# Optimization experiments

Hardware: AMD Instinct MI355X
Metric: run time of the kernel (lower is better)

## Reference

```python
import jax, jax.numpy as jnp
import numpy as np

HALF = 24576          # per-side HalfKP features (64 king sq * 6 piece * 64 sq)
NUMEL = 2 * HALF      # util.half_kp_numel()
BASE = 128
B = 8192


def _linear(x, W, b):
    return x @ W.T + b


def setup_inputs() -> dict:
    key = jax.random.key(0)
    ks = jax.random.split(key, 16)
    s = 0.01
    return {
        "pov": jax.random.uniform(ks[0], (B, 1), dtype=jnp.float32),
        "white": jax.random.uniform(ks[1], (B, HALF), dtype=jnp.float32),
        "black": jax.random.uniform(ks[2], (B, HALF), dtype=jnp.float32),
        "w_aff_W": jax.random.normal(ks[3], (BASE, NUMEL), dtype=jnp.float32) * s,
        "w_aff_b": jax.random.normal(ks[4], (BASE,), dtype=jnp.float32) * s,
        "b_aff_W": jax.random.normal(ks[5], (BASE, NUMEL), dtype=jnp.float32) * s,
        "b_aff_b": jax.random.normal(ks[6], (BASE,), dtype=jnp.float32) * s,
        "fc0_W": jax.random.normal(ks[7], (32, 2 * BASE), dtype=jnp.float32) * s,
        "fc0_b": jax.random.normal(ks[8], (32,), dtype=jnp.float32) * s,
        "fc1_W": jax.random.normal(ks[9], (32, 32), dtype=jnp.float32) * s,
        "fc1_b": jax.random.normal(ks[10], (32,), dtype=jnp.float32) * s,
        "fc2_W": jax.random.normal(ks[11], (32, 64), dtype=jnp.float32) * s,
        "fc2_b": jax.random.normal(ks[12], (32,), dtype=jnp.float32) * s,
        "fc3_W": jax.random.normal(ks[13], (1, 96), dtype=jnp.float32) * s,
        "fc3_b": jax.random.normal(ks[14], (1,), dtype=jnp.float32) * s,
    }


def reference(pov, white, black, w_aff_W, w_aff_b, b_aff_W, b_aff_b,
              fc0_W, fc0_b, fc1_W, fc1_b, fc2_W, fc2_b, fc3_W, fc3_b):
    # util.half_kp(a, b) = cat([a, b], dim=1)
    w_feat = jnp.concatenate([white, black], axis=1)  # [B, NUMEL]
    b_feat = jnp.concatenate([black, white], axis=1)
    w_ = _linear(w_feat, w_aff_W, w_aff_b)            # [B, 128]
    b_ = _linear(b_feat, b_aff_W, b_aff_b)
    wb = jnp.concatenate([w_, b_], axis=1)            # [B, 256]
    bw = jnp.concatenate([b_, w_], axis=1)
    base = jax.nn.relu(pov * wb + (1.0 - pov) * bw)
    x = jax.nn.relu(_linear(base, fc0_W, fc0_b))      # [B, 32]
    x = jnp.concatenate([x, jax.nn.relu(_linear(x, fc1_W, fc1_b))], axis=1)  # [B, 64]
    x = jnp.concatenate([x, jax.nn.relu(_linear(x, fc2_W, fc2_b))], axis=1)  # [B, 96]
    return _linear(x, fc3_W, fc3_b)                   # [B, 1]
```

## Files before the change

kernel.cpp:

```cpp
#include <hip/hip_runtime.h>
#include <hip/hip_bf16.h>
#include <stdint.h>

typedef float f32x4 __attribute__((ext_vector_type(4)));
typedef float fvec4 __attribute__((ext_vector_type(4)));
typedef short bf16x8 __attribute__((ext_vector_type(8)));
typedef short bf16x4 __attribute__((ext_vector_type(4)));

#define HALF_K 24576
#define NUMELK 49152
#define BATCH  8192
#define BM 128
#define BN 256
#define BK 64

__device__ __forceinline__ short f2bf(float f) {
  __hip_bfloat16 h = __float2bfloat16(f);
  return __builtin_bit_cast(short, h);
}

__device__ __forceinline__ void gload_lds16(const short* g, short* l) {
  __builtin_amdgcn_global_load_lds(
      (const __attribute__((address_space(1))) unsigned*)g,
      (__attribute__((address_space(3))) unsigned*)l, 16, 0, 0);
}

__global__ __launch_bounds__(256)
void nnue_prep(const float* __restrict__ wW, const float* __restrict__ bW,
               short* __restrict__ Bprep) {
  int gid = blockIdx.x * 256 + threadIdx.x;
  int KT  = gid >> 11;
  int rem = gid & 2047;
  int col = rem >> 3;
  int kc  = rem & 7;
  int kg  = KT * 64 + kc * 8;
  const float* src;
  if (col < 128) {
    src = wW + (size_t)col * NUMELK + kg;
  } else {
    int kk = (kg < HALF_K) ? (kg + HALF_K) : (kg - HALF_K);
    src = bW + (size_t)(col - 128) * NUMELK + kk;
  }
  fvec4 v0 = ((const fvec4*)src)[0];
  fvec4 v1 = ((const fvec4*)src)[1];
  bf16x8 o;
  o[0] = f2bf(v0[0]); o[1] = f2bf(v0[1]); o[2] = f2bf(v0[2]); o[3] = f2bf(v0[3]);
  o[4] = f2bf(v1[0]); o[5] = f2bf(v1[1]); o[6] = f2bf(v1[2]); o[7] = f2bf(v1[3]);
  *(bf16x8*)(Bprep + (size_t)KT * 16384 + col * 64 + ((kc ^ (col & 7)) << 3)) = o;
}

__global__ __launch_bounds__(512, 4)
void nnue_gemm(const float* __restrict__ white, const float* __restrict__ black,
               const short* __restrict__ Bprep, float* __restrict__ partial,
               int kchunk, int S) {
  __shared__ short A0s[BM * BK];
  __shared__ short A1s[BM * BK];
  __shared__ short Bls[BN * BK];

  const int t    = threadIdx.x;
  const int lane = t & 63;
  const int wid  = t >> 6;

  const int bid = blockIdx.x;
  const int xcd = bid & 7, bi = bid >> 3;
  const int xpk = 8 / S;
  const int ks  = xcd / xpk;
  const int mt  = (xcd % xpk) * (64 / xpk) + bi;
  const int m0  = mt * BM;
  const int k0  = ks * kchunk;
  const int KT0 = k0 / BK;

  f32x4 acc[4][4];
  const f32x4 zero = {0.f, 0.f, 0.f, 0.f};
#pragma unroll
  for (int a = 0; a < 4; ++a)
#pragma unroll
    for (int b = 0; b < 4; ++b) acc[a][b] = zero;

  const int wm = wid >> 2, wn = wid & 3;
  const int l15 = lane & 15, l4 = lane >> 4;

  const int rbase  = t >> 4;
  const int cchunk = t & 15;
  const size_t a_off = (size_t)(m0 + rbase) * HALF_K + cchunk * 4;
  const int swz    = ((cchunk >> 1) ^ (rbase & 7)) << 3;
  const int halfsh = (cchunk & 1) * 4;

  fvec4 va[4];

  auto issueA = [&](int kg) {
    const float* Af; int ka;
    if (kg < HALF_K) { Af = white; ka = kg; } else { Af = black; ka = kg - HALF_K; }
    const float* base = Af + a_off + ka;
#pragma unroll
    for (int j = 0; j < 4; ++j)
      va[j] = *(const fvec4*)(base + (size_t)32 * j * HALF_K);
  };

  auto issueB = [&](int KT) {
    const short* src = Bprep + (size_t)KT * 16384 + wid * 2048 + lane * 8;
    short* dst = &Bls[wid * 2048];
#pragma unroll
    for (int j = 0; j < 4; ++j)
      gload_lds16(src + j * 512, dst + j * 512);
  };

  auto writeA = [&](short* Ad) {
#pragma unroll
    for (int j = 0; j < 4; ++j) {
      int row = 32 * j + rbase;
      bf16x4 o;
      o[0] = f2bf(va[j][0]); o[1] = f2bf(va[j][1]);
      o[2] = f2bf(va[j][2]); o[3] = f2bf(va[j][3]);
      *(bf16x4*)&Ad[row * 64 + swz + halfsh] = o;
    }
  };

  auto compute = [&](const short* Ab) {
#pragma unroll
    for (int kstep = 0; kstep < 2; ++kstep) {
      const int kc = kstep * 4 + l4;
      bf16x8 bfr[4];
#pragma unroll
      for (int nf = 0; nf < 4; ++nf) {
        int col = wn * 64 + nf * 16 + l15;
        bfr[nf] = *(const bf16x8*)&Bls[col * 64 + ((kc ^ (col & 7)) << 3)];
      }
#pragma unroll
      for (int mf = 0; mf < 4; ++mf) {
        int row = wm * 64 + mf * 16 + l15;
        bf16x8 af = *(const bf16x8*)&Ab[row * 64 + ((kc ^ (row & 7)) << 3)];
#pragma unroll
        for (int nf = 0; nf < 4; ++nf)
          acc[mf][nf] = __builtin_amdgcn_mfma_f32_16x16x32_bf16(af, bfr[nf], acc[mf][nf], 0, 0, 0);
      }
    }
  };

  const int niter = kchunk / BK;

  issueA(k0);
  issueB(KT0);
  writeA(A0s);
  asm volatile("s_waitcnt lgkmcnt(0)" ::: "memory");

  for (int kt = 0; kt < niter; ++kt) {
    const bool hn = (kt + 1 < niter);
    short* Acur = (kt & 1) ? A1s : A0s;
    short* Anxt = (kt & 1) ? A0s : A1s;

    if (hn) {
      issueA(k0 + (kt + 1) * BK);
      asm volatile("s_waitcnt vmcnt(8)" ::: "memory");
    } else {
      asm volatile("s_waitcnt vmcnt(0)" ::: "memory");
    }
    __builtin_amdgcn_sched_barrier(0);
    __builtin_amdgcn_s_barrier();
    __builtin_amdgcn_sched_barrier(0);

    __builtin_amdgcn_s_setprio(1);
    compute(Acur);
    __builtin_amdgcn_s_setprio(0);

    __builtin_amdgcn_sched_barrier(0);
    __builtin_amdgcn_s_barrier();
    if (hn) {
      issueB(KT0 + kt + 1);
      writeA(Anxt);
      asm volatile("s_waitcnt lgkmcnt(0)" ::: "memory");
    }
  }

  float* P = partial + ((size_t)ks * BATCH + m0) * 256;
#pragma unroll
  for (int mf = 0; mf < 4; ++mf) {
    int row = wm * 64 + mf * 16 + l4 * 4;
#pragma unroll
    for (int nf = 0; nf < 4; ++nf) {
      int col = wn * 64 + nf * 16 + l15;
#pragma unroll
      for (int rr = 0; rr < 4; ++rr)
        P[(size_t)(row + rr) * 256 + col] = acc[mf][nf][rr];
    }
  }
}

__global__ __launch_bounds__(256)
void nnue_tail(const float* __restrict__ partial, int S,
               const float* __restrict__ pov,
               const float* __restrict__ waffb, const float* __restrict__ baffb,
               const float* __restrict__ fc0W, const float* __restrict__ fc0b,
               const float* __restrict__ fc1W, const float* __restrict__ fc1b,
               const float* __restrict__ fc2W, const float* __restrict__ fc2b,
               const float* __restrict__ fc3W, const float* __restrict__ fc3b,
               float* __restrict__ out) {
  __shared__ float w0s[32 * 256];
  __shared__ float w1s[32 * 32];
  __shared__ float w2s[32 * 64];
  __shared__ float w3s[96];
  __shared__ float b0s[32], b1s[32], b2s[32];
  __shared__ float base_s[4][256];
  __shared__ float b3s;

  const int t = threadIdx.x;
  for (int i = t; i < 8192; i += 256) { int j = i >> 8, k = i & 255; w0s[(j << 8) | ((k + j) & 255)] = fc0W[i]; }
  for (int i = t; i < 1024; i += 256) { int j = i >> 5, k = i & 31;  w1s[(j << 5) | ((k + j) & 31)]  = fc1W[i]; }
  for (int i = t; i < 2048; i += 256) { int j = i >> 6, k = i & 63;  w2s[(j << 6) | ((k + j) & 63)]  = fc2W[i]; }
  if (t < 96) w3s[t] = fc3W[t];
  if (t < 32) { b0s[t] = fc0b[t]; b1s[t] = fc1b[t]; b2s[t] = fc2b[t]; }
  if (t == 0) b3s = fc3b[0];
  __syncthreads();

  const int wid = t >> 6, lane = t & 63;
  const int m = blockIdx.x * 4 + wid;
  const float pv = pov[m];

  float val[4];
  {
    const float* p = partial + (size_t)m * 256 + lane * 4;
    fvec4 a = *(const fvec4*)p;
    for (int s = 1; s < S; ++s) a += *(const fvec4*)(p + (size_t)s * BATCH * 256);
    const int c0 = lane * 4;
#pragma unroll
    for (int j = 0; j < 4; ++j) {
      int c = c0 + j;
      float bias = (c < 128) ? waffb[c] : baffb[c - 128];
      val[j] = a[j] + bias;
    }
  }
#pragma unroll
  for (int j = 0; j < 4; ++j) {
    float other = __shfl(val[j], lane ^ 32, 64);
    if (lane < 32) {
      int c = lane * 4 + j;
      float w = val[j], b = other;
      base_s[wid][c]       = fmaxf(pv * w + (1.f - pv) * b, 0.f);
      base_s[wid][c + 128] = fmaxf(pv * b + (1.f - pv) * w, 0.f);
    }
  }
  __syncthreads();

  const int j = lane & 31, half = lane >> 5;
  const float* bs = &base_s[wid][0];

  float s0 = 0.f;
  for (int k = 0; k < 128; ++k) {
    int kk = half * 128 + k;
    s0 += bs[kk] * w0s[(j << 8) | ((kk + j) & 255)];
  }
  s0 += __shfl(s0, lane ^ 32, 64);
  float x0 = fmaxf(s0 + b0s[j], 0.f);

  float s1 = 0.f;
  for (int k = 0; k < 32; ++k)
    s1 += __shfl(x0, k, 64) * w1s[(j << 5) | ((k + j) & 31)];
  float x1 = fmaxf(s1 + b1s[j], 0.f);

  float s2 = 0.f;
  for (int k = 0; k < 32; ++k) {
    s2 += __shfl(x0, k, 64) * w2s[(j << 6) | ((k + j) & 63)];
    s2 += __shfl(x1, k, 64) * w2s[(j << 6) | ((k + 32 + j) & 63)];
  }
  float x2 = fmaxf(s2 + b2s[j], 0.f);

  float s3 = 0.f;
  for (int k = 0; k < 32; ++k) {
    s3 += __shfl(x0, k, 64) * w3s[k];
    s3 += __shfl(x1, k, 64) * w3s[32 + k];
    s3 += __shfl(x2, k, 64) * w3s[64 + k];
  }
  if (lane == 0) out[m] = s3 + b3s;
}

extern "C" void kernel_launch(void* const* d_in, const int* in_sizes, int n_in,
                              void* d_out, int out_size, void* d_ws, size_t ws_size,
                              hipStream_t stream) {
  const float* pov   = (const float*)d_in[0];
  const float* white = (const float*)d_in[1];
  const float* black = (const float*)d_in[2];
  const float* wW    = (const float*)d_in[3];
  const float* wb    = (const float*)d_in[4];
  const float* bW    = (const float*)d_in[5];
  const float* bb    = (const float*)d_in[6];
  const float* fc0W  = (const float*)d_in[7];
  const float* fc0b  = (const float*)d_in[8];
  const float* fc1W  = (const float*)d_in[9];
  const float* fc1b  = (const float*)d_in[10];
  const float* fc2W  = (const float*)d_in[11];
  const float* fc2b  = (const float*)d_in[12];
  const float* fc3W  = (const float*)d_in[13];
  const float* fc3b  = (const float*)d_in[14];
  float* out = (float*)d_out;

  short* Bprep = (short*)d_ws;
  const size_t BWS_BYTES = (size_t)256 * NUMELK * 2;
  float* partial = (float*)((char*)d_ws + BWS_BYTES);
  const size_t PART1 = (size_t)BATCH * 256 * 4;

  int S = 8;
  if (ws_size < BWS_BYTES + 8 * PART1) S = 4;
  if (ws_size < BWS_BYTES + 4 * PART1) S = 2;
  if (ws_size < BWS_BYTES + 2 * PART1) S = 1;

  nnue_prep<<<dim3(6144), 256, 0, stream>>>(wW, bW, Bprep);
  nnue_gemm<<<dim3(64 * S), 512, 0, stream>>>(white, black, Bprep, partial, NUMELK / S, S);
  nnue_tail<<<dim3(BATCH / 4), 256, 0, stream>>>(partial, S, pov, wb, bb,
      fc0W, fc0b, fc1W, fc1b, fc2W, fc2b, fc3W, fc3b, out);
}
```

Baseline: 445.6 us.

## Load B fragments directly from global memory and halve GEMM block rows

The GEMM no longer stages the preprocessed weight tile in shared memory. Each wave now reads its B fragments straight from global memory (the prep layout already matches the fragment pattern), and the block shrinks to 64 rows and 4 waves, doubling the grid. This removes the B LDS traffic, the async LDS loads and their waits, and frees LDS for occupancy. In exchange, B is reread from global/L2 by twice as many blocks, and global-load latency sits just before the MFMAs.

Result: slower. 570.5 us (+28.0%).

```diff
diff --git a/kernel.cpp b/kernel.cpp
--- a/kernel.cpp
+++ b/kernel.cpp
@@ -10,19 +10,13 @@
 #define HALF_K 24576
 #define NUMELK 49152
 #define BATCH  8192
-#define BM 128
+#define BM 64
 #define BN 256
 #define BK 64
 
 __device__ __forceinline__ short f2bf(float f) {
   __hip_bfloat16 h = __float2bfloat16(f);
   return __builtin_bit_cast(short, h);
-}
-
-__device__ __forceinline__ void gload_lds16(const short* g, short* l) {
-  __builtin_amdgcn_global_load_lds(
-      (const __attribute__((address_space(1))) unsigned*)g,
-      (__attribute__((address_space(3))) unsigned*)l, 16, 0, 0);
 }
 
 __global__ __launch_bounds__(256)
@@ -49,23 +43,22 @@
   *(bf16x8*)(Bprep + (size_t)KT * 16384 + col * 64 + ((kc ^ (col & 7)) << 3)) = o;
 }
 
-__global__ __launch_bounds__(512, 4)
+__global__ __launch_bounds__(256, 4)
 void nnue_gemm(const float* __restrict__ white, const float* __restrict__ black,
                const short* __restrict__ Bprep, float* __restrict__ partial,
                int kchunk, int S) {
   __shared__ short A0s[BM * BK];
   __shared__ short A1s[BM * BK];
-  __shared__ short Bls[BN * BK];
 
   const int t    = threadIdx.x;
   const int lane = t & 63;
-  const int wid  = t >> 6;
+  const int wn   = t >> 6;
 
   const int bid = blockIdx.x;
   const int xcd = bid & 7, bi = bid >> 3;
   const int xpk = 8 / S;
   const int ks  = xcd / xpk;
-  const int mt  = (xcd % xpk) * (64 / xpk) + bi;
+  const int mt  = (xcd % xpk) * (128 / xpk) + bi;
   const int m0  = mt * BM;
   const int k0  = ks * kchunk;
   const int KT0 = k0 / BK;
@@ -77,15 +70,12 @@
 #pragma unroll
     for (int b = 0; b < 4; ++b) acc[a][b] = zero;
 
-  const int wm = wid >> 2, wn = wid & 3;
   const int l15 = lane & 15, l4 = lane >> 4;
 
-  const int rbase  = t >> 4;
-  const int cchunk = t & 15;
-  const size_t a_off = (size_t)(m0 + rbase) * HALF_K + cchunk * 4;
-  const int swz    = ((cchunk >> 1) ^ (rbase & 7)) << 3;
-  const int halfsh = (cchunk & 1) * 4;
-
+  const int rbase = t >> 4;
+  const int chunk = t & 15;
+  const size_t a_off = (size_t)(m0 + rbase) * HALF_K + chunk * 4;
+  const int aswz = (((chunk >> 1) ^ (rbase & 7)) << 3) + (chunk & 1) * 4;
   fvec4 va[4];
 
   auto issueA = [&](int kg) {
@@ -94,88 +84,66 @@
     const float* base = Af + a_off + ka;
 #pragma unroll
     for (int j = 0; j < 4; ++j)
-      va[j] = *(const fvec4*)(base + (size_t)32 * j * HALF_K);
+      va[j] = *(const fvec4*)(base + (size_t)16 * j * HALF_K);
   };
 
-  auto issueB = [&](int KT) {
-    const short* src = Bprep + (size_t)KT * 16384 + wid * 2048 + lane * 8;
-    short* dst = &Bls[wid * 2048];
-#pragma unroll
-    for (int j = 0; j < 4; ++j)
-      gload_lds16(src + j * 512, dst + j * 512);
-  };
-
   auto writeA = [&](short* Ad) {
 #pragma unroll
     for (int j = 0; j < 4; ++j) {
-      int row = 32 * j + rbase;
       bf16x4 o;
       o[0] = f2bf(va[j][0]); o[1] = f2bf(va[j][1]);
       o[2] = f2bf(va[j][2]); o[3] = f2bf(va[j][3]);
-      *(bf16x4*)&Ad[row * 64 + swz + halfsh] = o;
+      *(bf16x4*)&Ad[(rbase + 16 * j) * 64 + aswz] = o;
     }
   };
 
-  auto compute = [&](const short* Ab) {
+  const int bvar0 = (l15 * 64 + ((l4)     ^ (l15 & 7)) * 8) * 2;
+  const int bvar1 = (l15 * 64 + ((4 + l4) ^ (l15 & 7)) * 8) * 2;
+
+  const int niter = kchunk / BK;
+
+  issueA(k0);
+  writeA(A0s);
+  __syncthreads();
+
+  for (int kt = 0; kt < niter; ++kt) {
+    const bool hn = (kt + 1 < niter);
+    const short* Acur = (kt & 1) ? A1s : A0s;
+    short* Anxt = (kt & 1) ? A0s : A1s;
+
+    const char* bp = (const char*)(Bprep + (size_t)(KT0 + kt) * 16384 + wn * 4096);
+    bf16x8 bfr[2][4];
+#pragma unroll
+    for (int nf = 0; nf < 4; ++nf)
+      bfr[0][nf] = *(const bf16x8*)(bp + nf * 2048 + bvar0);
+#pragma unroll
+    for (int nf = 0; nf < 4; ++nf)
+      bfr[1][nf] = *(const bf16x8*)(bp + nf * 2048 + bvar1);
+    if (hn) issueA(k0 + (kt + 1) * BK);
+    __builtin_amdgcn_sched_barrier(0);
+
 #pragma unroll
     for (int kstep = 0; kstep < 2; ++kstep) {
       const int kc = kstep * 4 + l4;
-      bf16x8 bfr[4];
-#pragma unroll
-      for (int nf = 0; nf < 4; ++nf) {
-        int col = wn * 64 + nf * 16 + l15;
-        bfr[nf] = *(const bf16x8*)&Bls[col * 64 + ((kc ^ (col & 7)) << 3)];
+#pragma unroll
+      for (int mf = 0; mf < 4; ++mf) {
+        int row = mf * 16 + l15;
+        bf16x8 af = *(const bf16x8*)&Acur[row * 64 + ((kc ^ (row & 7)) << 3)];
+#pragma unroll
+        for (int nf = 0; nf < 4; ++nf)
+          acc[mf][nf] = __builtin_amdgcn_mfma_f32_16x16x32_bf16(af, bfr[kstep][nf], acc[mf][nf], 0, 0, 0);
       }
-#pragma unroll
-      for (int mf = 0; mf < 4; ++mf) {
-        int row = wm * 64 + mf * 16 + l15;
-        bf16x8 af = *(const bf16x8*)&Ab[row * 64 + ((kc ^ (row & 7)) << 3)];
-#pragma unroll
-        for (int nf = 0; nf < 4; ++nf)
-          acc[mf][nf] = __builtin_amdgcn_mfma_f32_16x16x32_bf16(af, bfr[nf], acc[mf][nf], 0, 0, 0);
-      }
-    }
-  };
-
-  const int niter = kchunk / BK;
-
-  issueA(k0);
-  issueB(KT0);
-  writeA(A0s);
-  asm volatile("s_waitcnt lgkmcnt(0)" ::: "memory");
-
-  for (int kt = 0; kt < niter; ++kt) {
-    const bool hn = (kt + 1 < niter);
-    short* Acur = (kt & 1) ? A1s : A0s;
-    short* Anxt = (kt & 1) ? A0s : A1s;
-
-    if (hn) {
-      issueA(k0 + (kt + 1) * BK);
-      asm volatile("s_waitcnt vmcnt(8)" ::: "memory");
-    } else {
-      asm volatile("s_waitcnt vmcnt(0)" ::: "memory");
     }
     __builtin_amdgcn_sched_barrier(0);
-    __builtin_amdgcn_s_barrier();
-    __builtin_amdgcn_sched_barrier(0);
-
-    __builtin_amdgcn_s_setprio(1);
-    compute(Acur);
-    __builtin_amdgcn_s_setprio(0);
-
-    __builtin_amdgcn_sched_barrier(0);
-    __builtin_amdgcn_s_barrier();
-    if (hn) {
-      issueB(KT0 + kt + 1);
-      writeA(Anxt);
-      asm volatile("s_waitcnt lgkmcnt(0)" ::: "memory");
-    }
+
+    if (hn) writeA(Anxt);
+    __syncthreads();
   }
 
   float* P = partial + ((size_t)ks * BATCH + m0) * 256;
 #pragma unroll
   for (int mf = 0; mf < 4; ++mf) {
-    int row = wm * 64 + mf * 16 + l4 * 4;
+    int row = mf * 16 + l4 * 4;
 #pragma unroll
     for (int nf = 0; nf < 4; ++nf) {
       int col = wn * 64 + nf * 16 + l15;
@@ -304,7 +272,7 @@
   if (ws_size < BWS_BYTES + 2 * PART1) S = 1;
 
   nnue_prep<<<dim3(6144), 256, 0, stream>>>(wW, bW, Bprep);
-  nnue_gemm<<<dim3(64 * S), 512, 0, stream>>>(white, black, Bprep, partial, NUMELK / S, S);
+  nnue_gemm<<<dim3(128 * S), 256, 0, stream>>>(white, black, Bprep, partial, NUMELK / S, S);
   nnue_tail<<<dim3(BATCH / 4), 256, 0, stream>>>(partial, S, pov, wb, bb,
       fc0W, fc0b, fc1W, fc1b, fc2W, fc2b, fc3W, fc3b, out);
 }
```
